# Kernel optimization log

Hardware: AMD Instinct MI355X
Metric: run time of the kernel (lower is better)

The kernel has to match this reference:

```python
import jax, jax.numpy as jnp
import numpy as np

N = 100000      # nodes
E = 1600000     # edges (avg degree 16)
IN = 128        # input_dim
H = 8           # heads
D = 8           # hidden_dim (== heads, required by the diversity-loss bmm)
HD = H * D      # per-layer width
OUT = 10        # output_dim
G = 64          # graphs in batch
NEG = 0.2       # GATConv leaky_relu slope
DIVW = 0.1      # diversity_weight


def setup_inputs() -> dict:
    key = jax.random.key(0)
    ks = jax.random.split(key, 20)
    w = lambda k, shape, fan: (jax.random.normal(k, shape, jnp.float32) / np.sqrt(fan)).astype(jnp.float32)
    inp = {}
    inp['x'] = jax.random.normal(ks[0], (N, IN), jnp.float32)
    inp['edge_index'] = jax.random.randint(ks[1], (2, E), 0, N, dtype=jnp.int32)
    inp['batch'] = jnp.sort(jax.random.randint(ks[2], (N,), 0, G, dtype=jnp.int32))
    # layer 0: GATConv(IN -> D, heads=H)
    inp['W0'] = w(ks[3], (IN, HD), IN)
    inp['att_src0'] = w(ks[4], (H, D), D)
    inp['att_dst0'] = w(ks[5], (H, D), D)
    inp['b0'] = jnp.zeros((HD,), jnp.float32)
    inp['gamma0'] = jnp.ones((HD,), jnp.float32)
    inp['beta0'] = jnp.zeros((HD,), jnp.float32)
    inp['P0'] = w(ks[6], (H, D), D)
    # layer 1: GATConv(HD -> D, heads=H)
    inp['W1'] = w(ks[7], (HD, HD), HD)
    inp['att_src1'] = w(ks[8], (H, D), D)
    inp['att_dst1'] = w(ks[9], (H, D), D)
    inp['b1'] = jnp.zeros((HD,), jnp.float32)
    inp['gamma1'] = jnp.ones((HD,), jnp.float32)
    inp['beta1'] = jnp.zeros((HD,), jnp.float32)
    inp['P1'] = w(ks[10], (H, D), D)
    inp['fc_W'] = w(ks[11], (HD, OUT), HD)
    inp['fc_b'] = jnp.zeros((OUT,), jnp.float32)
    return inp


def _gat(x, src, dst, W, a_src, a_dst, b):
    h = (x @ W).reshape(-1, H, D)                       # [N,H,D]
    al = jnp.sum(h * a_src, -1)                          # [N,H] src scores
    ar = jnp.sum(h * a_dst, -1)                          # [N,H] dst scores
    e = jax.nn.leaky_relu(al[src] + ar[dst], NEG)        # [E,H]
    m = jax.ops.segment_max(e, dst, num_segments=N)      # per-dst max (stable softmax)
    m = jnp.where(jnp.isfinite(m), m, 0.0)
    ex = jnp.exp(e - m[dst])
    den = jax.ops.segment_sum(ex, dst, num_segments=N)
    a = ex / (den[dst] + 1e-16)                          # PyG softmax eps
    out = jax.ops.segment_sum(a[:, :, None] * h[src], dst, num_segments=N)  # [N,H,D]
    return out.reshape(-1, HD) + b


def _bn(x, g, b):  # BatchNorm1d, training-mode batch stats, eps=1e-5
    mu = x.mean(0)
    var = x.var(0)
    return g * (x - mu) * jax.lax.rsqrt(var + 1e-5) + b


def _div_loss(x, P):
    xr = x.reshape(-1, H, D)
    pr = jnp.einsum('nij,jk->nik', xr, P)                # bmm with shared projector (needs D==H)
    nh = pr / jnp.maximum(jnp.linalg.norm(pr, axis=-1, keepdims=True), 1e-8)
    S = jnp.einsum('nid,njd->ij', nh, nh) / x.shape[0]   # mean-over-nodes cosine sims [H,H]
    iu = jnp.triu_indices(H, 1)
    return jnp.mean(S[iu] ** 2)


def reference(x, edge_index, batch, W0, att_src0, att_dst0, b0, gamma0, beta0, P0,
              W1, att_src1, att_dst1, b1, gamma1, beta1, P1, fc_W, fc_b):
    src, dst = edge_index[0], edge_index[1]
    dl = 0.0
    h = _gat(x, src, dst, W0, att_src0, att_dst0, b0)
    dl = dl + _div_loss(h, P0)
    h = jax.nn.elu(_bn(h, gamma0, beta0))
    h = _gat(h, src, dst, W1, att_src1, att_dst1, b1)
    dl = dl + _div_loss(h, P1)
    h = jax.nn.elu(_bn(h, gamma1, beta1))
    cnt = jax.ops.segment_sum(jnp.ones((N,), h.dtype), batch, num_segments=G)
    pooled = jax.ops.segment_sum(h, batch, num_segments=G) / jnp.maximum(cnt, 1.0)[:, None]
    logits = pooled @ fc_W + fc_b
    return logits, DIVW * dl
```

## Files before the change

kernel.cpp:

```cpp
#include <hip/hip_runtime.h>
#include <hip/hip_fp16.h>

#define NB 100000
#define NE 1600000
#define PSH 12500
#define BCAP 64
#define SCB 2048
#define GMB 1568
#define MIXB 3136

typedef int iv4 __attribute__((ext_vector_type(4)));

__device__ __forceinline__ float elu_f(float x) { return x > 0.f ? x : expm1f(x); }

__global__ __launch_bounds__(256) void k_fill_zero(float4* __restrict__ p, int n4) {
    int i = blockIdx.x * 256 + threadIdx.x, s = gridDim.x * 256;
    float4 z = make_float4(0.f, 0.f, 0.f, 0.f);
    for (; i < n4; i += s) p[i] = z;
}

__global__ __launch_bounds__(256) void k_scat_gemm(
    const iv4* __restrict__ src4, const iv4* __restrict__ dst4,
    int* __restrict__ cnt, int* __restrict__ buck, int ne4,
    const float* __restrict__ X, const float* __restrict__ W,
    const float* __restrict__ attS, const float* __restrict__ attD,
    __half* __restrict__ Hout, float* __restrict__ al, float* __restrict__ ar, int nrows)
{
    __shared__ float4 xs4[64][16];
    __shared__ float  ws_[64][64];
    int b = blockIdx.x, t = threadIdx.x;
    int isS, idx;
    if (b < MIXB) {
        int g = b >> 3;
        isS = g & 1;
        idx = (g >> 1) * 8 + (b & 7);
    } else {
        isS = 1;
        idx = GMB + (b - MIXB);
    }

    if (isS) {
        int part = idx & 7;
        unsigned lo = part * PSH;
        int pb = idx >> 3;
        int st = (SCB >> 3) * 256;
        int i  = pb * 256 + t;
        int i2 = i + st;
        int st2 = st * 2;
        for (; i2 < ne4; i += st2, i2 += st2) {
            iv4 dA = dst4[i];
            iv4 dB = dst4[i2];
            bool ax = (unsigned)(dA.x - lo) < PSH;
            bool ay = (unsigned)(dA.y - lo) < PSH;
            bool az = (unsigned)(dA.z - lo) < PSH;
            bool aw = (unsigned)(dA.w - lo) < PSH;
            bool bx = (unsigned)(dB.x - lo) < PSH;
            bool by = (unsigned)(dB.y - lo) < PSH;
            bool bz = (unsigned)(dB.z - lo) < PSH;
            bool bw = (unsigned)(dB.w - lo) < PSH;
            bool anyA = ax | ay | az | aw;
            bool anyB = bx | by | bz | bw;
            if (!(anyA | anyB)) continue;
            iv4 sA, sB;
            if (anyA) sA = src4[i];
            if (anyB) sB = src4[i2];
            int pax, pay, paz, paw, pbx, pby, pbz, pbw;
            if (ax) pax = atomicAdd(&cnt[dA.x], 1);
            if (ay) pay = atomicAdd(&cnt[dA.y], 1);
            if (az) paz = atomicAdd(&cnt[dA.z], 1);
            if (aw) paw = atomicAdd(&cnt[dA.w], 1);
            if (bx) pbx = atomicAdd(&cnt[dB.x], 1);
            if (by) pby = atomicAdd(&cnt[dB.y], 1);
            if (bz) pbz = atomicAdd(&cnt[dB.z], 1);
            if (bw) pbw = atomicAdd(&cnt[dB.w], 1);
            if (ax) buck[(dA.x << 6) + (pax & (BCAP - 1))] = sA.x;
            if (ay) buck[(dA.y << 6) + (pay & (BCAP - 1))] = sA.y;
            if (az) buck[(dA.z << 6) + (paz & (BCAP - 1))] = sA.z;
            if (aw) buck[(dA.w << 6) + (paw & (BCAP - 1))] = sA.w;
            if (bx) buck[(dB.x << 6) + (pbx & (BCAP - 1))] = sB.x;
            if (by) buck[(dB.y << 6) + (pby & (BCAP - 1))] = sB.y;
            if (bz) buck[(dB.z << 6) + (pbz & (BCAP - 1))] = sB.z;
            if (bw) buck[(dB.w << 6) + (pbw & (BCAP - 1))] = sB.w;
        }
        if (i < ne4) {
            iv4 d = dst4[i];
            bool cx = (unsigned)(d.x - lo) < PSH;
            bool cy = (unsigned)(d.y - lo) < PSH;
            bool cz = (unsigned)(d.z - lo) < PSH;
            bool cw = (unsigned)(d.w - lo) < PSH;
            if (cx | cy | cz | cw) {
                iv4 s = src4[i];
                if (cx) buck[(d.x << 6) + (atomicAdd(&cnt[d.x], 1) & (BCAP - 1))] = s.x;
                if (cy) buck[(d.y << 6) + (atomicAdd(&cnt[d.y], 1) & (BCAP - 1))] = s.y;
                if (cz) buck[(d.z << 6) + (atomicAdd(&cnt[d.z], 1) & (BCAP - 1))] = s.z;
                if (cw) buck[(d.w << 6) + (atomicAdd(&cnt[d.w], 1) & (BCAP - 1))] = s.w;
            }
        }
        return;
    }

    int rowBase = idx * 64;
    int r = t & 63, cg = t >> 6, c0 = cg * 16;
    float acc[16];
#pragma unroll
    for (int j = 0; j < 16; ++j) acc[j] = 0.f;
    int sw = r & 15;

    for (int kc = 0; kc < 2; ++kc) {
        if (kc) __syncthreads();
        for (int i = t; i < 1024; i += 256)
            ((float4*)ws_)[i] = ((const float4*)W)[kc * 1024 + i];
        for (int i = t; i < 1024; i += 256) {
            int rr = i >> 4, c4 = i & 15;
            int gr = rowBase + rr;
            float4 v = make_float4(0.f, 0.f, 0.f, 0.f);
            if (gr < nrows) v = ((const float4*)X)[gr * 32 + kc * 16 + c4];
            xs4[rr][c4 ^ (rr & 15)] = v;
        }
        __syncthreads();
        for (int k4 = 0; k4 < 16; ++k4) {
            float4 xv = xs4[r][k4 ^ sw];
            float xk[4] = {xv.x, xv.y, xv.z, xv.w};
#pragma unroll
            for (int kk = 0; kk < 4; ++kk) {
                const float* wrow = &ws_[k4 * 4 + kk][c0];
                float4 wa = *(const float4*)(wrow + 0);
                float4 wb = *(const float4*)(wrow + 4);
                float4 wc = *(const float4*)(wrow + 8);
                float4 wd = *(const float4*)(wrow + 12);
                float x = xk[kk];
                acc[0]  += x * wa.x; acc[1]  += x * wa.y; acc[2]  += x * wa.z; acc[3]  += x * wa.w;
                acc[4]  += x * wb.x; acc[5]  += x * wb.y; acc[6]  += x * wb.z; acc[7]  += x * wb.w;
                acc[8]  += x * wc.x; acc[9]  += x * wc.y; acc[10] += x * wc.z; acc[11] += x * wc.w;
                acc[12] += x * wd.x; acc[13] += x * wd.y; acc[14] += x * wd.z; acc[15] += x * wd.w;
            }
        }
    }

    int gr = rowBase + r;
    if (gr < nrows) {
        __half2 hp[8];
#pragma unroll
        for (int j = 0; j < 8; ++j) hp[j] = __floats2half2_rn(acc[2 * j], acc[2 * j + 1]);
        uint4* op = (uint4*)(Hout + (size_t)gr * 64 + c0);
        op[0] = *(uint4*)&hp[0];
        op[1] = *(uint4*)&hp[4];
#pragma unroll
        for (int hh = 0; hh < 2; ++hh) {
            int h = cg * 2 + hh;
            float sa = 0.f, sd = 0.f;
#pragma unroll
            for (int d = 0; d < 8; ++d) {
                float hv = acc[hh * 8 + d];
                sa += hv * attS[h * 8 + d];
                sd += hv * attD[h * 8 + d];
            }
            al[gr * 8 + h] = sa;
            ar[gr * 8 + h] = sd;
        }
    }
}

__global__ __launch_bounds__(256) void k_gemm1(
    const float* __restrict__ X, const float* __restrict__ W,
    const float* __restrict__ attS, const float* __restrict__ attD,
    const float* __restrict__ bsum, const float* __restrict__ bsq,
    const float* __restrict__ gamma, const float* __restrict__ beta,
    __half* __restrict__ Hout, float* __restrict__ al, float* __restrict__ ar, int nrows)
{
    __shared__ float4 xs4[64][16];
    __shared__ float  ws_[64][64];
    __shared__ float  sc_[64], sh_[64];
    int t = threadIdx.x;
    int rowBase = blockIdx.x * 64;
    if (t < 64) {
        float invn = 1.f / (float)NB;
        float mu = bsum[t] * invn;
        float var = bsq[t] * invn - mu * mu;
        float s = gamma[t] * rsqrtf(var + 1e-5f);
        sc_[t] = s;
        sh_[t] = beta[t] - mu * s;
    }
    for (int i = t; i < 1024; i += 256)
        ((float4*)ws_)[i] = ((const float4*)W)[i];
    __syncthreads();

    for (int i = t; i < 1024; i += 256) {
        int rr = i >> 4, c4 = i & 15;
        int gr = rowBase + rr;
        float4 v = make_float4(0.f, 0.f, 0.f, 0.f);
        if (gr < nrows) v = ((const float4*)X)[gr * 16 + c4];
        int c = c4 * 4;
        v.x = elu_f(sc_[c + 0] * v.x + sh_[c + 0]);
        v.y = elu_f(sc_[c + 1] * v.y + sh_[c + 1]);
        v.z = elu_f(sc_[c + 2] * v.z + sh_[c + 2]);
        v.w = elu_f(sc_[c + 3] * v.w + sh_[c + 3]);
        xs4[rr][c4 ^ (rr & 15)] = v;
    }
    __syncthreads();

    int r = t & 63, cg = t >> 6, c0 = cg * 16;
    float acc[16];
#pragma unroll
    for (int j = 0; j < 16; ++j) acc[j] = 0.f;
    int sw = r & 15;
    for (int k4 = 0; k4 < 16; ++k4) {
        float4 xv = xs4[r][k4 ^ sw];
        float xk[4] = {xv.x, xv.y, xv.z, xv.w};
#pragma unroll
        for (int kk = 0; kk < 4; ++kk) {
            const float* wrow = &ws_[k4 * 4 + kk][c0];
            float4 wa = *(const float4*)(wrow + 0);
            float4 wb = *(const float4*)(wrow + 4);
            float4 wc = *(const float4*)(wrow + 8);
            float4 wd = *(const float4*)(wrow + 12);
            float x = xk[kk];
            acc[0]  += x * wa.x; acc[1]  += x * wa.y; acc[2]  += x * wa.z; acc[3]  += x * wa.w;
            acc[4]  += x * wb.x; acc[5]  += x * wb.y; acc[6]  += x * wb.z; acc[7]  += x * wb.w;
            acc[8]  += x * wc.x; acc[9]  += x * wc.y; acc[10] += x * wc.z; acc[11] += x * wc.w;
            acc[12] += x * wd.x; acc[13] += x * wd.y; acc[14] += x * wd.z; acc[15] += x * wd.w;
        }
    }
    int gr = rowBase + r;
    if (gr < nrows) {
        __half2 hp[8];
#pragma unroll
        for (int j = 0; j < 8; ++j) hp[j] = __floats2half2_rn(acc[2 * j], acc[2 * j + 1]);
        uint4* op = (uint4*)(Hout + (size_t)gr * 64 + c0);
        op[0] = *(uint4*)&hp[0];
        op[1] = *(uint4*)&hp[4];
#pragma unroll
        for (int hh = 0; hh < 2; ++hh) {
            int h = cg * 2 + hh;
            float sa = 0.f, sd = 0.f;
#pragma unroll
            for (int d = 0; d < 8; ++d) {
                float hv = acc[hh * 8 + d];
                sa += hv * attS[h * 8 + d];
                sd += hv * attD[h * 8 + d];
            }
            al[gr * 8 + h] = sa;
            ar[gr * 8 + h] = sd;
        }
    }
}

__global__ __launch_bounds__(256) void k_agg(const int* __restrict__ cnt, const int* __restrict__ buck,
    const float* __restrict__ al, const float* __restrict__ ar,
    const __half* __restrict__ Hf, const float* __restrict__ bias,
    float* __restrict__ agg, int n)
{
    int lane = threadIdx.x & 63;
    int w  = __builtin_amdgcn_readfirstlane((blockIdx.x * 256 + (int)threadIdx.x) >> 6);
    int nw = (gridDim.x * 256) >> 6;
    int h = lane >> 3;
    float bl = bias[lane];
    for (int d = w; d < n; d += nw) {
        int r0 = d << 6;
        int r1 = r0 + __builtin_amdgcn_readfirstlane(cnt[d]);
        float arh = ar[d * 8 + h];
        float ac0 = 0.f, ac1 = 0.f, ac2 = 0.f, ac3 = 0.f, ac4 = 0.f, ac5 = 0.f, ac6 = 0.f, ac7 = 0.f;
        float de0 = 0.f, de1 = 0.f, de2 = 0.f, de3 = 0.f, de4 = 0.f, de5 = 0.f, de6 = 0.f, de7 = 0.f;
        int p = r0;
        for (; p + 8 <= r1; p += 8) {
            int s0 = __builtin_amdgcn_readfirstlane(buck[p]);
            int s1 = __builtin_amdgcn_readfirstlane(buck[p + 1]);
            int s2 = __builtin_amdgcn_readfirstlane(buck[p + 2]);
            int s3 = __builtin_amdgcn_readfirstlane(buck[p + 3]);
            int s4 = __builtin_amdgcn_readfirstlane(buck[p + 4]);
            int s5 = __builtin_amdgcn_readfirstlane(buck[p + 5]);
            int s6 = __builtin_amdgcn_readfirstlane(buck[p + 6]);
            int s7 = __builtin_amdgcn_readfirstlane(buck[p + 7]);
            float t0 = al[s0 * 8 + h] + arh;
            float t1 = al[s1 * 8 + h] + arh;
            float t2 = al[s2 * 8 + h] + arh;
            float t3 = al[s3 * 8 + h] + arh;
            float t4 = al[s4 * 8 + h] + arh;
            float t5 = al[s5 * 8 + h] + arh;
            float t6 = al[s6 * 8 + h] + arh;
            float t7 = al[s7 * 8 + h] + arh;
            float h0 = __half2float(Hf[((size_t)s0 << 6) + lane]);
            float h1 = __half2float(Hf[((size_t)s1 << 6) + lane]);
            float h2 = __half2float(Hf[((size_t)s2 << 6) + lane]);
            float h3 = __half2float(Hf[((size_t)s3 << 6) + lane]);
            float h4 = __half2float(Hf[((size_t)s4 << 6) + lane]);
            float h5 = __half2float(Hf[((size_t)s5 << 6) + lane]);
            float h6 = __half2float(Hf[((size_t)s6 << 6) + lane]);
            float h7 = __half2float(Hf[((size_t)s7 << 6) + lane]);
            t0 = t0 > 0.f ? t0 : 0.2f * t0;  t1 = t1 > 0.f ? t1 : 0.2f * t1;
            t2 = t2 > 0.f ? t2 : 0.2f * t2;  t3 = t3 > 0.f ? t3 : 0.2f * t3;
            t4 = t4 > 0.f ? t4 : 0.2f * t4;  t5 = t5 > 0.f ? t5 : 0.2f * t5;
            t6 = t6 > 0.f ? t6 : 0.2f * t6;  t7 = t7 > 0.f ? t7 : 0.2f * t7;
            float e0 = __expf(t0), e1 = __expf(t1), e2 = __expf(t2), e3 = __expf(t3);
            float e4 = __expf(t4), e5 = __expf(t5), e6 = __expf(t6), e7 = __expf(t7);
            de0 += e0; ac0 = fmaf(e0, h0, ac0);
            de1 += e1; ac1 = fmaf(e1, h1, ac1);
            de2 += e2; ac2 = fmaf(e2, h2, ac2);
            de3 += e3; ac3 = fmaf(e3, h3, ac3);
            de4 += e4; ac4 = fmaf(e4, h4, ac4);
            de5 += e5; ac5 = fmaf(e5, h5, ac5);
            de6 += e6; ac6 = fmaf(e6, h6, ac6);
            de7 += e7; ac7 = fmaf(e7, h7, ac7);
        }
        for (; p + 4 <= r1; p += 4) {
            int s0 = __builtin_amdgcn_readfirstlane(buck[p]);
            int s1 = __builtin_amdgcn_readfirstlane(buck[p + 1]);
            int s2 = __builtin_amdgcn_readfirstlane(buck[p + 2]);
            int s3 = __builtin_amdgcn_readfirstlane(buck[p + 3]);
            float t0 = al[s0 * 8 + h] + arh;
            float t1 = al[s1 * 8 + h] + arh;
            float t2 = al[s2 * 8 + h] + arh;
            float t3 = al[s3 * 8 + h] + arh;
            float h0 = __half2float(Hf[((size_t)s0 << 6) + lane]);
            float h1 = __half2float(Hf[((size_t)s1 << 6) + lane]);
            float h2 = __half2float(Hf[((size_t)s2 << 6) + lane]);
            float h3 = __half2float(Hf[((size_t)s3 << 6) + lane]);
            t0 = t0 > 0.f ? t0 : 0.2f * t0;  t1 = t1 > 0.f ? t1 : 0.2f * t1;
            t2 = t2 > 0.f ? t2 : 0.2f * t2;  t3 = t3 > 0.f ? t3 : 0.2f * t3;
            float e0 = __expf(t0), e1 = __expf(t1), e2 = __expf(t2), e3 = __expf(t3);
            de0 += e0; ac0 = fmaf(e0, h0, ac0);
            de1 += e1; ac1 = fmaf(e1, h1, ac1);
            de2 += e2; ac2 = fmaf(e2, h2, ac2);
            de3 += e3; ac3 = fmaf(e3, h3, ac3);
        }
        for (; p < r1; ++p) {
            int s0 = __builtin_amdgcn_readfirstlane(buck[p]);
            float t0 = al[s0 * 8 + h] + arh;
            float h0 = __half2float(Hf[((size_t)s0 << 6) + lane]);
            t0 = t0 > 0.f ? t0 : 0.2f * t0;
            float e0 = __expf(t0);
            de0 += e0; ac0 = fmaf(e0, h0, ac0);
        }
        float den = ((de0 + de1) + (de2 + de3)) + ((de4 + de5) + (de6 + de7));
        float num = ((ac0 + ac1) + (ac2 + ac3)) + ((ac4 + ac5) + (ac6 + ac7));
        float inv = 1.f / (den + 1e-16f);
        agg[(size_t)d * 64 + lane] = fmaf(num, inv, bl);
    }
}

__global__ __launch_bounds__(256) void k_post(const float* __restrict__ agg, const float* __restrict__ P,
    float* __restrict__ Sord, float* __restrict__ bsum, float* __restrict__ bsq, int n)
{
    __shared__ float Ps[64];
    __shared__ float red[4][184];
    int t = threadIdx.x;
    if (t < 64) Ps[t] = P[t];
    __syncthreads();
    int lane = t & 63, wid = t >> 6;
    int h = lane & 7, grp = lane >> 3;
    int w  = (blockIdx.x * 256 + t) >> 6;
    int nw = (gridDim.x * 256) >> 6;
    float sacc[7], bs[8], bq[8];
#pragma unroll
    for (int i = 0; i < 7; ++i) sacc[i] = 0.f;
#pragma unroll
    for (int i = 0; i < 8; ++i) { bs[i] = 0.f; bq[i] = 0.f; }

    for (int base = w * 8; base < n; base += nw * 8) {
        int node = base + grp;
        float xv[8];
        if (node < n) {
            const float4* rp = (const float4*)(agg + (size_t)node * 64 + h * 8);
            float4 a = rp[0], b = rp[1];
            xv[0]=a.x; xv[1]=a.y; xv[2]=a.z; xv[3]=a.w; xv[4]=b.x; xv[5]=b.y; xv[6]=b.z; xv[7]=b.w;
        } else {
#pragma unroll
            for (int k = 0; k < 8; ++k) xv[k] = 0.f;
        }
#pragma unroll
        for (int k = 0; k < 8; ++k) { bs[k] += xv[k]; bq[k] += xv[k] * xv[k]; }
        float pr[8];
#pragma unroll
        for (int k = 0; k < 8; ++k) pr[k] = 0.f;
#pragma unroll
        for (int j = 0; j < 8; ++j) {
            float x = xv[j];
#pragma unroll
            for (int k = 0; k < 8; ++k) pr[k] += x * Ps[j * 8 + k];
        }
        float nrm2 = 0.f;
#pragma unroll
        for (int k = 0; k < 8; ++k) nrm2 += pr[k] * pr[k];
        float inv = 1.f / fmaxf(sqrtf(nrm2), 1e-8f);
#pragma unroll
        for (int k = 0; k < 8; ++k) pr[k] *= inv;
#pragma unroll
        for (int d = 1; d < 8; ++d) {
            float dot = 0.f;
#pragma unroll
            for (int k = 0; k < 8; ++k) dot += pr[k] * __shfl_xor(pr[k], d, 64);
            sacc[d - 1] += dot;
        }
    }
#pragma unroll
    for (int d = 0; d < 7; ++d) {
        sacc[d] += __shfl_xor(sacc[d], 8, 64);
        sacc[d] += __shfl_xor(sacc[d], 16, 64);
        sacc[d] += __shfl_xor(sacc[d], 32, 64);
    }
#pragma unroll
    for (int k = 0; k < 8; ++k) {
        bs[k] += __shfl_xor(bs[k], 8, 64); bs[k] += __shfl_xor(bs[k], 16, 64); bs[k] += __shfl_xor(bs[k], 32, 64);
        bq[k] += __shfl_xor(bq[k], 8, 64); bq[k] += __shfl_xor(bq[k], 16, 64); bq[k] += __shfl_xor(bq[k], 32, 64);
    }
    if (lane < 8) {
#pragma unroll
        for (int d = 0; d < 7; ++d) red[wid][h * 23 + d] = sacc[d];
#pragma unroll
        for (int k = 0; k < 8; ++k) { red[wid][h * 23 + 7 + k] = bs[k]; red[wid][h * 23 + 15 + k] = bq[k]; }
    }
    __syncthreads();
    if (t < 184) {
        float v = red[0][t] + red[1][t] + red[2][t] + red[3][t];
        int hh = t / 23, r = t % 23;
        if (r < 7)       atomicAdd(&Sord[hh * 8 + (hh ^ (r + 1))], v);
        else if (r < 15) atomicAdd(&bsum[hh * 8 + (r - 7)], v);
        else             atomicAdd(&bsq [hh * 8 + (r - 15)], v);
    }
}

__global__ __launch_bounds__(256) void k_pool(const float* __restrict__ agg, const int* __restrict__ batch,
    const float* __restrict__ bsum, const float* __restrict__ bsq,
    const float* __restrict__ gamma, const float* __restrict__ beta,
    float* __restrict__ psum, float* __restrict__ cnt, int n)
{
    int lane = threadIdx.x & 63;
    int w  = (blockIdx.x * 256 + threadIdx.x) >> 6;
    int nw = (gridDim.x * 256) >> 6;
    int chunk = (n + nw - 1) / nw;
    int n0 = w * chunk;
    if (n0 >= n) return;
    int n1 = min(n, n0 + chunk);
    float invn = 1.f / (float)n;
    float mu = bsum[lane] * invn;
    float var = bsq[lane] * invn - mu * mu;
    float sc = gamma[lane] * rsqrtf(var + 1e-5f);
    float sh = beta[lane] - mu * sc;
    float acc = 0.f;
    int curg = batch[n0], run = 0;
    for (int i = n0; i < n1; ++i) {
        int g = batch[i];
        if (g != curg) {
            atomicAdd(psum + curg * 64 + lane, acc);
            if (lane == 0) atomicAdd(cnt + curg, (float)run);
            acc = 0.f; run = 0; curg = g;
        }
        float v = agg[(size_t)i * 64 + lane];
        v = sc * v + sh;
        v = v > 0.f ? v : expm1f(v);
        acc += v; run += 1;
    }
    atomicAdd(psum + curg * 64 + lane, acc);
    if (lane == 0) atomicAdd(cnt + curg, (float)run);
}

__global__ __launch_bounds__(640) void k_final(const float* __restrict__ psum, const float* __restrict__ cnt,
    const float* __restrict__ fcW, const float* __restrict__ fcb,
    const float* __restrict__ S0, const float* __restrict__ S1,
    float* __restrict__ out, int n)
{
    __shared__ float pl[64][65];
    int t = threadIdx.x;
    for (int i = t; i < 4096; i += 640) {
        int g = i >> 6, c = i & 63;
        pl[g][c] = psum[i] / fmaxf(cnt[g], 1.f);
    }
    __syncthreads();
    {
        int g = t / 10, o = t % 10;
        float s = fcb[o];
#pragma unroll 8
        for (int c = 0; c < 64; ++c) s += pl[g][c] * fcW[c * 10 + o];
        out[g * 10 + o] = s;
    }
    if (t == 0) {
        float invn = 1.f / (float)n;
        float dl = 0.f;
        for (int i = 0; i < 8; ++i)
            for (int j = i + 1; j < 8; ++j) {
                float v0 = S0[i * 8 + j] * invn; dl += v0 * v0;
                float v1 = S1[i * 8 + j] * invn; dl += v1 * v1;
            }
        out[640] = 0.1f * (dl / 28.f);
    }
}

extern "C" void kernel_launch(void* const* d_in, const int* in_sizes, int n_in,
                              void* d_out, int out_size, void* d_ws, size_t ws_size,
                              hipStream_t stream)
{
    const float* x   = (const float*)d_in[0];
    const int*   ei  = (const int*)d_in[1];
    const int*   bat = (const int*)d_in[2];
    const float* W0  = (const float*)d_in[3];
    const float* as0 = (const float*)d_in[4];
    const float* ad0 = (const float*)d_in[5];
    const float* b0  = (const float*)d_in[6];
    const float* g0  = (const float*)d_in[7];
    const float* be0 = (const float*)d_in[8];
    const float* P0  = (const float*)d_in[9];
    const float* W1  = (const float*)d_in[10];
    const float* as1 = (const float*)d_in[11];
    const float* ad1 = (const float*)d_in[12];
    const float* b1  = (const float*)d_in[13];
    const float* g1  = (const float*)d_in[14];
    const float* be1 = (const float*)d_in[15];
    const float* P1  = (const float*)d_in[16];
    const float* fcW = (const float*)d_in[17];
    const float* fcb = (const float*)d_in[18];
    const int* src = ei;
    const int* dst = ei + NE;

    float* ws    = (float*)d_ws;
    __half* Hbuf = (__half*)ws;
    float* agg   = ws + 6400000;
    float* al    = ws + 12800000;
    float* ar    = ws + 13600000;
    float* stats = ws + 14400000;
    float* psum  = ws + 14401024;
    int*   cnt   = (int*)(ws + 14405120);
    int*   buck  = cnt + NB;

    float* Sord0 = stats + 0;
    float* Sord1 = stats + 64;
    float* sum0  = stats + 128;
    float* sq0   = stats + 192;
    float* sum1  = stats + 256;
    float* sq1   = stats + 320;
    float* gcnt  = stats + 640;

    k_fill_zero<<<103, 256, 0, stream>>>((float4*)stats, 26280);

    k_scat_gemm<<<SCB + GMB, 256, 0, stream>>>((const iv4*)src, (const iv4*)dst, cnt, buck, NE / 4,
                                               x, W0, as0, ad0, Hbuf, al, ar, NB);

    k_agg<<<25000, 256, 0, stream>>>(cnt, buck, al, ar, Hbuf, b0, agg, NB);
    k_post<<<512, 256, 0, stream>>>(agg, P0, Sord0, sum0, sq0, NB);

    k_gemm1<<<1563, 256, 0, stream>>>(agg, W1, as1, ad1, sum0, sq0, g0, be0, Hbuf, al, ar, NB);
    k_agg<<<25000, 256, 0, stream>>>(cnt, buck, al, ar, Hbuf, b1, agg, NB);
    k_post<<<512, 256, 0, stream>>>(agg, P1, Sord1, sum1, sq1, NB);

    k_pool<<<512, 256, 0, stream>>>(agg, bat, sum1, sq1, g1, be1, psum, gcnt, NB);
    k_final<<<1, 640, 0, stream>>>(psum, gcnt, fcW, fcb, Sord0, Sord1, (float*)d_out, NB);
}
```

Baseline: 325.9 us.

## Compute attention exps once per edge-head and broadcast via bpermute in aggregation

Restructures the aggregation kernel so each wavefront loads 8 neighbor indices at once, with each lane computing one (edge, head) score and exp. The exp weights are then broadcast to the feature lanes with ds_bpermute, and neighbor indices are read with readlane. This removes the 8x redundant al loads and exp evaluations per edge that the old layout performed across the lanes sharing a head. In exchange it adds cross-lane permute traffic and a shuffle reduction for the denominator. It also clamps the degree to BCAP and the indices to the valid node range.

```diff
diff --git a/kernel.cpp b/kernel.cpp
--- a/kernel.cpp
+++ b/kernel.cpp
@@ -253,88 +253,62 @@
     int lane = threadIdx.x & 63;
     int w  = __builtin_amdgcn_readfirstlane((blockIdx.x * 256 + (int)threadIdx.x) >> 6);
     int nw = (gridDim.x * 256) >> 6;
-    int h = lane >> 3;
+    int eidx = lane >> 3;
+    int hs   = lane & 7;
+    int hb   = lane >> 3;
+    int bpbase = hb * 4;
     float bl = bias[lane];
     for (int d = w; d < n; d += nw) {
+        int deg = __builtin_amdgcn_readfirstlane(cnt[d]);
+        deg = deg < BCAP ? deg : BCAP;
         int r0 = d << 6;
-        int r1 = r0 + __builtin_amdgcn_readfirstlane(cnt[d]);
-        float arh = ar[d * 8 + h];
-        float ac0 = 0.f, ac1 = 0.f, ac2 = 0.f, ac3 = 0.f, ac4 = 0.f, ac5 = 0.f, ac6 = 0.f, ac7 = 0.f;
-        float de0 = 0.f, de1 = 0.f, de2 = 0.f, de3 = 0.f, de4 = 0.f, de5 = 0.f, de6 = 0.f, de7 = 0.f;
-        int p = r0;
-        for (; p + 8 <= r1; p += 8) {
-            int s0 = __builtin_amdgcn_readfirstlane(buck[p]);
-            int s1 = __builtin_amdgcn_readfirstlane(buck[p + 1]);
-            int s2 = __builtin_amdgcn_readfirstlane(buck[p + 2]);
-            int s3 = __builtin_amdgcn_readfirstlane(buck[p + 3]);
-            int s4 = __builtin_amdgcn_readfirstlane(buck[p + 4]);
-            int s5 = __builtin_amdgcn_readfirstlane(buck[p + 5]);
-            int s6 = __builtin_amdgcn_readfirstlane(buck[p + 6]);
-            int s7 = __builtin_amdgcn_readfirstlane(buck[p + 7]);
-            float t0 = al[s0 * 8 + h] + arh;
-            float t1 = al[s1 * 8 + h] + arh;
-            float t2 = al[s2 * 8 + h] + arh;
-            float t3 = al[s3 * 8 + h] + arh;
-            float t4 = al[s4 * 8 + h] + arh;
-            float t5 = al[s5 * 8 + h] + arh;
-            float t6 = al[s6 * 8 + h] + arh;
-            float t7 = al[s7 * 8 + h] + arh;
-            float h0 = __half2float(Hf[((size_t)s0 << 6) + lane]);
-            float h1 = __half2float(Hf[((size_t)s1 << 6) + lane]);
-            float h2 = __half2float(Hf[((size_t)s2 << 6) + lane]);
-            float h3 = __half2float(Hf[((size_t)s3 << 6) + lane]);
-            float h4 = __half2float(Hf[((size_t)s4 << 6) + lane]);
-            float h5 = __half2float(Hf[((size_t)s5 << 6) + lane]);
-            float h6 = __half2float(Hf[((size_t)s6 << 6) + lane]);
-            float h7 = __half2float(Hf[((size_t)s7 << 6) + lane]);
-            t0 = t0 > 0.f ? t0 : 0.2f * t0;  t1 = t1 > 0.f ? t1 : 0.2f * t1;
-            t2 = t2 > 0.f ? t2 : 0.2f * t2;  t3 = t3 > 0.f ? t3 : 0.2f * t3;
-            t4 = t4 > 0.f ? t4 : 0.2f * t4;  t5 = t5 > 0.f ? t5 : 0.2f * t5;
-            t6 = t6 > 0.f ? t6 : 0.2f * t6;  t7 = t7 > 0.f ? t7 : 0.2f * t7;
-            float e0 = __expf(t0), e1 = __expf(t1), e2 = __expf(t2), e3 = __expf(t3);
-            float e4 = __expf(t4), e5 = __expf(t5), e6 = __expf(t6), e7 = __expf(t7);
-            de0 += e0; ac0 = fmaf(e0, h0, ac0);
-            de1 += e1; ac1 = fmaf(e1, h1, ac1);
-            de2 += e2; ac2 = fmaf(e2, h2, ac2);
-            de3 += e3; ac3 = fmaf(e3, h3, ac3);
-            de4 += e4; ac4 = fmaf(e4, h4, ac4);
-            de5 += e5; ac5 = fmaf(e5, h5, ac5);
-            de6 += e6; ac6 = fmaf(e6, h6, ac6);
-            de7 += e7; ac7 = fmaf(e7, h7, ac7);
-        }
-        for (; p + 4 <= r1; p += 4) {
-            int s0 = __builtin_amdgcn_readfirstlane(buck[p]);
-            int s1 = __builtin_amdgcn_readfirstlane(buck[p + 1]);
-            int s2 = __builtin_amdgcn_readfirstlane(buck[p + 2]);
-            int s3 = __builtin_amdgcn_readfirstlane(buck[p + 3]);
-            float t0 = al[s0 * 8 + h] + arh;
-            float t1 = al[s1 * 8 + h] + arh;
-            float t2 = al[s2 * 8 + h] + arh;
-            float t3 = al[s3 * 8 + h] + arh;
-            float h0 = __half2float(Hf[((size_t)s0 << 6) + lane]);
-            float h1 = __half2float(Hf[((size_t)s1 << 6) + lane]);
-            float h2 = __half2float(Hf[((size_t)s2 << 6) + lane]);
-            float h3 = __half2float(Hf[((size_t)s3 << 6) + lane]);
-            t0 = t0 > 0.f ? t0 : 0.2f * t0;  t1 = t1 > 0.f ? t1 : 0.2f * t1;
-            t2 = t2 > 0.f ? t2 : 0.2f * t2;  t3 = t3 > 0.f ? t3 : 0.2f * t3;
-            float e0 = __expf(t0), e1 = __expf(t1), e2 = __expf(t2), e3 = __expf(t3);
-            de0 += e0; ac0 = fmaf(e0, h0, ac0);
-            de1 += e1; ac1 = fmaf(e1, h1, ac1);
-            de2 += e2; ac2 = fmaf(e2, h2, ac2);
-            de3 += e3; ac3 = fmaf(e3, h3, ac3);
-        }
-        for (; p < r1; ++p) {
-            int s0 = __builtin_amdgcn_readfirstlane(buck[p]);
-            float t0 = al[s0 * 8 + h] + arh;
-            float h0 = __half2float(Hf[((size_t)s0 << 6) + lane]);
-            t0 = t0 > 0.f ? t0 : 0.2f * t0;
-            float e0 = __expf(t0);
-            de0 += e0; ac0 = fmaf(e0, h0, ac0);
-        }
-        float den = ((de0 + de1) + (de2 + de3)) + ((de4 + de5) + (de6 + de7));
-        float num = ((ac0 + ac1) + (ac2 + ac3)) + ((ac4 + ac5) + (ac6 + ac7));
+        float arh = ar[d * 8 + hs];
+        float den_sc = 0.f;
+        float acc0 = 0.f, acc1 = 0.f;
+        int nf = deg >> 3, tail = deg & 7;
+        int p = 0;
+        for (int it = 0; it < nf; ++it, p += 8) {
+            int vb = buck[r0 + p + eidx];
+            unsigned vbs = min((unsigned)vb, (unsigned)(NB - 1));
+            float tv = al[(size_t)vbs * 8 + hs] + arh;
+            tv = tv > 0.f ? tv : 0.2f * tv;
+            float ev = __expf(tv);
+            den_sc += ev;
+            int evi = __float_as_int(ev);
+#pragma unroll
+            for (int e = 0; e < 8; e += 2) {
+                unsigned s0 = min((unsigned)__builtin_amdgcn_readlane(vb, e * 8), (unsigned)(NB - 1));
+                unsigned s1 = min((unsigned)__builtin_amdgcn_readlane(vb, e * 8 + 8), (unsigned)(NB - 1));
+                float p0 = __int_as_float(__builtin_amdgcn_ds_bpermute(bpbase + e * 32, evi));
+                float p1 = __int_as_float(__builtin_amdgcn_ds_bpermute(bpbase + e * 32 + 32, evi));
+                float h0 = __half2float(Hf[((size_t)s0 << 6) + lane]);
+                float h1 = __half2float(Hf[((size_t)s1 << 6) + lane]);
+                acc0 = fmaf(p0, h0, acc0);
+                acc1 = fmaf(p1, h1, acc1);
+            }
+        }
+        if (tail) {
+            int vb = buck[r0 + p + eidx];
+            unsigned vbs = min((unsigned)vb, (unsigned)(NB - 1));
+            float tv = al[(size_t)vbs * 8 + hs] + arh;
+            tv = tv > 0.f ? tv : 0.2f * tv;
+            float ev = __expf(tv);
+            if (eidx >= tail) ev = 0.f;
+            den_sc += ev;
+            int evi = __float_as_int(ev);
+            for (int e = 0; e < tail; ++e) {
+                unsigned se = min((unsigned)__builtin_amdgcn_readlane(vb, e * 8), (unsigned)(NB - 1));
+                float pe = __int_as_float(__builtin_amdgcn_ds_bpermute(bpbase + e * 32, evi));
+                float hv = __half2float(Hf[((size_t)se << 6) + lane]);
+                acc0 = fmaf(pe, hv, acc0);
+            }
+        }
+        den_sc += __shfl_xor(den_sc, 8, 64);
+        den_sc += __shfl_xor(den_sc, 16, 64);
+        den_sc += __shfl_xor(den_sc, 32, 64);
+        float den = __shfl(den_sc, hb, 64);
         float inv = 1.f / (den + 1e-16f);
-        agg[(size_t)d * 64 + lane] = fmaf(num, inv, bl);
+        agg[(size_t)d * 64 + lane] = fmaf(acc0 + acc1, inv, bl);
     }
 }
 
```

New measurement: 345.2 us. 5.9% more time.
